# Kernel optimization log

Measured on AMD Instinct MI355X. Metric: run time of the kernel, lower is better.

The kernel has to match this reference:

```python
import jax, jax.numpy as jnp
import numpy as np
import math

B, T, D, H = 4, 1024, 1024, 16
DK = D // H
TAU_THRESH = 0.3


def setup_inputs() -> dict:
    key = jax.random.key(0)
    ks = jax.random.split(key, 13)
    s = 1.0 / math.sqrt(D)
    return {
        "x": jax.random.normal(ks[0], (B, T, D), dtype=jnp.float32),
        "Wq": jax.random.normal(ks[1], (D, D), dtype=jnp.float32) * s,
        "bq": jax.random.normal(ks[2], (D,), dtype=jnp.float32) * s,
        "Wk": jax.random.normal(ks[3], (D, D), dtype=jnp.float32) * s,
        "bk": jax.random.normal(ks[4], (D,), dtype=jnp.float32) * s,
        "Wv": jax.random.normal(ks[5], (D, D), dtype=jnp.float32) * s,
        "bv": jax.random.normal(ks[6], (D,), dtype=jnp.float32) * s,
        "Wo": jax.random.normal(ks[7], (D, D), dtype=jnp.float32) * s,
        "bo": jax.random.normal(ks[8], (D,), dtype=jnp.float32) * s,
        "Wg1": jax.random.normal(ks[9], (1, D), dtype=jnp.float32) * s,
        "bg1": jax.random.normal(ks[10], (1,), dtype=jnp.float32) * s,
        "Wg2": jax.random.normal(ks[11], (1, D), dtype=jnp.float32) * s,
        "bg2": jax.random.normal(ks[12], (1,), dtype=jnp.float32) * s,
    }


def reference(x, Wq, bq, Wk, bk, Wv, bv, Wo, bo, Wg1, bg1, Wg2, bg2):
    b, t, d = x.shape
    # projections (torch Linear: y = x @ W.T + b)
    Q = (x @ Wq.T + bq).reshape(b, t, H, DK).transpose(0, 2, 1, 3)  # [B,H,T,dk]
    K = (x @ Wk.T + bk).reshape(b, t, H, DK).transpose(0, 2, 1, 3)
    V = (x @ Wv.T + bv).reshape(b, t, H, DK).transpose(0, 2, 1, 3)
    scores = jnp.einsum("bhqd,bhkd->bhqk", Q, K) / math.sqrt(DK)  # [B,H,T,T]
    # confidence gates from first-token query context [B, H*dk] = [B, D]
    context = Q[:, :, 0, :].reshape(b, d)
    q1 = jax.nn.sigmoid(context @ Wg1.T + bg1)  # [B,1]
    q2 = jax.nn.sigmoid(context @ Wg2.T + bg2)  # [B,1]
    c = jnp.clip(q1 * q2, 1e-8, 1.0)            # [B,1]
    tau = jnp.where(c < TAU_THRESH, 1.0 / c, jnp.ones_like(c)).reshape(b, 1, 1, 1)
    p = jax.nn.softmax(scores / tau, axis=-1)
    cb = c.reshape(b, 1, 1, 1)
    p_gated = cb * p + (1.0 - cb) * (1.0 / t)
    u = jnp.mean(1.0 - c, axis=-1, keepdims=True)  # [B,1]
    attn_out = jnp.einsum("bhqk,bhkd->bhqd", p_gated, V)
    attn_out = attn_out.transpose(0, 2, 1, 3).reshape(b, t, d)
    output = attn_out @ Wo.T + bo
    return output, u
```

## Files before the change

kernel.cpp:

```cpp
#include <hip/hip_runtime.h>
#include <stdint.h>

typedef short bf16x8 __attribute__((ext_vector_type(8)));
typedef float f32x4 __attribute__((ext_vector_type(4)));

#define MFMA_BF16(a, b, c) __builtin_amdgcn_mfma_f32_16x16x32_bf16((a), (b), (c), 0, 0, 0)

__device__ __forceinline__ short f2bf(float x) {
  union { float f; uint32_t u; } v; v.f = x;
  uint32_t r = (v.u + 0x7FFFu + ((v.u >> 16) & 1u)) >> 16;
  return (short)r;
}
__device__ __forceinline__ uint32_t rnd_bf_hi(float x) {
  union { float f; uint32_t u; } v; v.f = x;
  return v.u + 0x7FFFu + ((v.u >> 16) & 1u);
}
__device__ __forceinline__ uint32_t pack2bf(float a, float b) {
  return __builtin_amdgcn_perm(rnd_bf_hi(b), rnd_bf_hi(a), 0x07060302);
}
__device__ __forceinline__ float bfbits2f(uint32_t b16) {
  union { uint32_t u; float f; } v; v.u = b16 << 16; return v.f;
}
__device__ __forceinline__ float fexp2(float x) {
#if __has_builtin(__builtin_amdgcn_exp2f)
  return __builtin_amdgcn_exp2f(x);
#else
  return __expf(x * 0.6931471805599453f);
#endif
}
__device__ __forceinline__ void async16(const void* g, void* l) {
  __builtin_amdgcn_global_load_lds(
      (const __attribute__((address_space(1))) uint32_t*)g,
      (__attribute__((address_space(3))) uint32_t*)l, 16, 0, 0);
}

#define BAR() __builtin_amdgcn_s_barrier()
#define LGKM0() asm volatile("s_waitcnt lgkmcnt(0)" ::: "memory")
#define VMCNT(n) asm volatile("s_waitcnt vmcnt(" #n ")" ::: "memory")
#define PRIO1() __builtin_amdgcn_s_setprio(1)
#define PRIO0() __builtin_amdgcn_s_setprio(0)

__global__ __launch_bounds__(256) void prep_k(
    const float* __restrict__ x, const float* __restrict__ Wq,
    const float* __restrict__ Wk, const float* __restrict__ Wv,
    const float* __restrict__ Wo, const float* __restrict__ bq,
    short* __restrict__ xb, short* __restrict__ Wqb, short* __restrict__ Wkb,
    short* __restrict__ Wvb, short* __restrict__ Wob, float* __restrict__ ctx) {
  __shared__ float xs[1024];
  const int bid = blockIdx.x;
  const int tid = threadIdx.x;
  if (bid < 8192) {
    const float* src; short* dst; int idx;
    if (bid < 4096) {
      src = x; dst = xb; idx = (bid << 8) + tid;
    } else {
      const int r = bid - 4096;
      const int z = r >> 10;
      src = (z == 0) ? Wq : (z == 1) ? Wk : (z == 2) ? Wv : Wo;
      dst = (z == 0) ? Wqb : (z == 1) ? Wkb : (z == 2) ? Wvb : Wob;
      idx = ((r & 1023) << 8) + tid;
    }
    float4 v = ((const float4*)src)[idx];
    short4 o;
    o.x = f2bf(v.x); o.y = f2bf(v.y); o.z = f2bf(v.z); o.w = f2bf(v.w);
    ((short4*)dst)[idx] = o;
  } else {
    const int r = bid - 8192;
    const int b = r >> 4;
    const int n0 = (r & 15) << 6;
    for (int i = tid; i < 1024; i += 256) xs[i] = x[b * 1048576 + i];
    __syncthreads();
    const int w = tid >> 6, lane = tid & 63;
    const float4* xv4 = (const float4*)xs;
    for (int rr = 0; rr < 16; ++rr) {
      const int n = n0 + (w << 4) + rr;
      const float4* wrow = (const float4*)(Wq + n * 1024);
      float p = 0.f;
#pragma unroll
      for (int c2 = 0; c2 < 4; ++c2) {
        float4 wv = wrow[lane + (c2 << 6)];
        float4 xv = xv4[lane + (c2 << 6)];
        p += xv.x * wv.x + xv.y * wv.y + xv.z * wv.z + xv.w * wv.w;
      }
#pragma unroll
      for (int off = 32; off; off >>= 1) p += __shfl_xor(p, off);
      if (lane == 0) ctx[b * 1024 + n] = p + bq[n];
    }
  }
}

__global__ __launch_bounds__(256) void gates_fin(const float* __restrict__ ctx,
                                                 const float* __restrict__ Wg1,
                                                 const float* __restrict__ bg1,
                                                 const float* __restrict__ Wg2,
                                                 const float* __restrict__ bg2,
                                                 float* __restrict__ gates,
                                                 float* __restrict__ u_out) {
  __shared__ float red[16];
  const int tid = threadIdx.x, w = tid >> 6, lane = tid & 63;
  for (int b = 0; b < 4; ++b) {
    float4 cv = ((const float4*)(ctx + b * 1024))[tid];
    float4 w1 = ((const float4*)Wg1)[tid];
    float4 w2 = ((const float4*)Wg2)[tid];
    float p1 = cv.x * w1.x + cv.y * w1.y + cv.z * w1.z + cv.w * w1.w;
    float p2 = cv.x * w2.x + cv.y * w2.y + cv.z * w2.z + cv.w * w2.w;
#pragma unroll
    for (int off = 32; off; off >>= 1) { p1 += __shfl_xor(p1, off); p2 += __shfl_xor(p2, off); }
    if (lane == 0) { red[w] = p1; red[8 + w] = p2; }
    __syncthreads();
    if (tid == 0) {
      float g1 = red[0] + red[1] + red[2] + red[3] + bg1[0];
      float g2 = red[8] + red[9] + red[10] + red[11] + bg2[0];
      float q1 = 1.f / (1.f + expf(-g1));
      float q2 = 1.f / (1.f + expf(-g2));
      float c = fminf(fmaxf(q1 * q2, 1e-8f), 1.0f);
      gates[b * 2 + 0] = c;
      gates[b * 2 + 1] = (c < 0.3f ? c : 1.0f) * 0.125f * 1.4426950408889634f;
      u_out[b] = 1.0f - c;
    }
    __syncthreads();
  }
}

template <bool SWP>
__device__ __forceinline__ void qkv_core(const short* __restrict__ xb,
                                         const short* __restrict__ W,
                                         const float* __restrict__ bias,
                                         short* __restrict__ out,
                                         short* sm, int m0, int nl0) {
  const int tid = threadIdx.x;
  const int wid = tid >> 6, lane = tid & 63;
  const int wr = wid >> 2, wc = wid & 3;
  const int m15 = lane & 15, quad = lane >> 4;
  const int swz = m15 & 7;

  const int rowb = tid >> 3;
  const int cs = ((tid & 7) ^ (rowb & 7)) << 3;
  const short* aB = xb + (m0 + rowb) * 1024 + cs;
  const short* bB = W + (nl0 + rowb) * 1024 + cs;

  short* As = sm;
  short* Bs = sm + 32768;

#define STAGEH(sb, tt, hf, dst)                        \
  do {                                                 \
    const short* _s = (sb) + (hf)*131072 + (tt)*64;    \
    short* _d = (dst) + ((hf) << 13) + (tid << 3);     \
    async16(_s, _d);                                   \
    async16(_s + 65536, _d + 4096);                    \
  } while (0)

#define RD(base, f, kk)                                                        \
  (*(const bf16x8*)((base) + ((f) << 10) + (m15 << 6) +                        \
                    (((((kk) << 2) + quad) ^ swz) << 3)))

#define MM(accr, af, bf)                                   \
  do {                                                     \
    if (SWP) accr = MFMA_BF16((bf), (af), (accr));         \
    else     accr = MFMA_BF16((af), (bf), (accr));         \
  } while (0)

  f32x4 acc[8][4];
#pragma unroll
  for (int i = 0; i < 8; ++i)
#pragma unroll
    for (int j = 0; j < 4; ++j) { f32x4 zz = {0.f, 0.f, 0.f, 0.f}; acc[i][j] = zz; }

  STAGEH(bB, 0, 0, Bs);
  STAGEH(aB, 0, 0, As);
  STAGEH(aB, 0, 1, As);
  STAGEH(bB, 0, 1, Bs);
  STAGEH(bB, 1, 0, Bs + 16384);
  STAGEH(aB, 1, 0, As + 16384);
  VMCNT(4);
  BAR();

  bf16x8 a[4][2], b0[2][2], b1[2][2];

  for (int t = 0; t < 16; ++t) {
    const int buf = t & 1;
    const short* Ab = As + (buf << 14) + (wr << 13);
    const short* Bb = Bs + (buf << 14) + ((wc >> 1) << 13) + ((wc & 1) << 12);
    short* Adn = As + ((buf ^ 1) << 14);
    short* Bdn = Bs + ((buf ^ 1) << 14);
    short* Ad2 = As + (buf << 14);
    short* Bd2 = Bs + (buf << 14);

#pragma unroll
    for (int fi = 0; fi < 4; ++fi) { a[fi][0] = RD(Ab, fi, 0); a[fi][1] = RD(Ab, fi, 1); }
#pragma unroll
    for (int fj = 0; fj < 2; ++fj) { b0[fj][0] = RD(Bb, fj, 0); b0[fj][1] = RD(Bb, fj, 1); }
    if (t < 15) STAGEH(aB, t + 1, 1, Adn);
    BAR();
    LGKM0();
    PRIO1();
#pragma unroll
    for (int fi = 0; fi < 4; ++fi)
#pragma unroll
      for (int fj = 0; fj < 2; ++fj) {
        MM(acc[fi][fj], a[fi][0], b0[fj][0]);
        MM(acc[fi][fj], a[fi][1], b0[fj][1]);
      }
    PRIO0();
    BAR();

#pragma unroll
    for (int fj = 0; fj < 2; ++fj) { b1[fj][0] = RD(Bb, 2 + fj, 0); b1[fj][1] = RD(Bb, 2 + fj, 1); }
    if (t < 15) STAGEH(bB, t + 1, 1, Bdn);
    BAR();
    LGKM0();
    PRIO1();
#pragma unroll
    for (int fi = 0; fi < 4; ++fi)
#pragma unroll
      for (int fj = 0; fj < 2; ++fj) {
        MM(acc[fi][2 + fj], a[fi][0], b1[fj][0]);
        MM(acc[fi][2 + fj], a[fi][1], b1[fj][1]);
      }
    PRIO0();
    BAR();

#pragma unroll
    for (int fi = 0; fi < 4; ++fi) { a[fi][0] = RD(Ab, 4 + fi, 0); a[fi][1] = RD(Ab, 4 + fi, 1); }
    if (t < 14) STAGEH(bB, t + 2, 0, Bd2);
    BAR();
    LGKM0();
    PRIO1();
#pragma unroll
    for (int fi = 0; fi < 4; ++fi)
#pragma unroll
      for (int fj = 0; fj < 2; ++fj) {
        MM(acc[4 + fi][2 + fj], a[fi][0], b1[fj][0]);
        MM(acc[4 + fi][2 + fj], a[fi][1], b1[fj][1]);
      }
    PRIO0();
    BAR();

    if (t < 14) STAGEH(aB, t + 2, 0, Ad2);
    BAR();
    PRIO1();
#pragma unroll
    for (int fi = 0; fi < 4; ++fi)
#pragma unroll
      for (int fj = 0; fj < 2; ++fj) {
        MM(acc[4 + fi][fj], a[fi][0], b0[fj][0]);
        MM(acc[4 + fi][fj], a[fi][1], b0[fj][1]);
      }
    PRIO0();
    if (t < 14) { VMCNT(4); }
    else if (t == 14) { VMCNT(0); }
    BAR();
  }

  const int nw = nl0 + (wc << 6);
  if (SWP) {
#pragma unroll
    for (int fj = 0; fj < 4; ++fj) {
      const int n = nw + (fj << 4) + (quad << 2);
      const float4 bv = *(const float4*)(bias + n);
      const int hh = n >> 6, dk0 = n & 63;
#pragma unroll
      for (int fi = 0; fi < 8; ++fi) {
        const int m = m0 + (wr << 7) + (fi << 4) + m15;
        const int bb = m >> 10, tt = m & 1023;
        uint2 st;
        st.x = pack2bf(acc[fi][fj][0] + bv.x, acc[fi][fj][1] + bv.y);
        st.y = pack2bf(acc[fi][fj][2] + bv.z, acc[fi][fj][3] + bv.w);
        *(uint2*)(out + (((bb << 4) + hh) << 16) + (tt << 6) + dk0) = st;
      }
    }
  } else {
#pragma unroll
    for (int fj = 0; fj < 4; ++fj) {
      const int n = nw + (fj << 4) + m15;
      const float bv = bias[n];
      const int hh = n >> 6, dk = n & 63;
#pragma unroll
      for (int fi = 0; fi < 8; ++fi) {
        const int m = m0 + (wr << 7) + (fi << 4) + (quad << 2);
        const int bb = m >> 10, t0 = m & 1023;
        uint2 st;
        st.x = pack2bf(acc[fi][fj][0] + bv, acc[fi][fj][1] + bv);
        st.y = pack2bf(acc[fi][fj][2] + bv, acc[fi][fj][3] + bv);
        *(uint2*)(out + (((bb << 4) + hh) << 16) + (dk << 10) + t0) = st;
      }
    }
  }
#undef STAGEH
#undef RD
#undef MM
}

__global__ __launch_bounds__(512) void gemm_qkv8(
    const short* __restrict__ xb,
    const short* __restrict__ Wqb, const short* __restrict__ Wkb, const short* __restrict__ Wvb,
    const float* __restrict__ bq, const float* __restrict__ bk, const float* __restrict__ bv,
    short* __restrict__ Qh, short* __restrict__ Kh, short* __restrict__ Vt) {
  const int lin = blockIdx.x;
  const int s = ((lin & 7) * 24) + (lin >> 3);
  const int bx = s & 15, by = s >> 4;
  const int z = by >> 2;
  const int m0 = bx << 8, nl0 = (by & 3) << 8;
  extern __shared__ short sm[];
  if (z == 0)      qkv_core<true >(xb, Wqb, bq, Qh, sm, m0, nl0);
  else if (z == 1) qkv_core<true >(xb, Wkb, bk, Kh, sm, m0, nl0);
  else             qkv_core<false>(xb, Wvb, bv, Vt, sm, m0, nl0);
}

__global__ __launch_bounds__(256) void gemm_out(const short* __restrict__ Ab,
                                                const short* __restrict__ Wo,
                                                const float* __restrict__ bo,
                                                float* __restrict__ Cout) {
  const int m0 = blockIdx.x << 6;
  const int n0 = blockIdx.y << 7;
  const int tid = threadIdx.x;
  const int w = tid >> 6, lane = tid & 63;
  const int m15 = lane & 15, quad = lane >> 4;
  const int wr = w >> 1, wc = w & 1;

  __shared__ short As[2048];
  __shared__ short Bs[4096];

  f32x4 acc[2][4];
#pragma unroll
  for (int i = 0; i < 2; ++i)
#pragma unroll
    for (int j = 0; j < 4; ++j) { f32x4 zz = {0.f, 0.f, 0.f, 0.f}; acc[i][j] = zz; }

  const int s0 = tid, s1 = tid + 256;
  const int arow = s0 >> 2, alcb = (s0 & 3) ^ ((arow >> 1) & 3);
  const int brow1 = s1 >> 2, blcb1 = (s1 & 3) ^ ((brow1 >> 1) & 3);
  const short* gA  = Ab + (m0 + arow) * 1024 + (alcb << 3);
  const short* gB0 = Wo + (n0 + arow) * 1024 + (alcb << 3);
  const short* gB1 = Wo + (n0 + brow1) * 1024 + (blcb1 << 3);
  short* lA  = &As[s0 << 3];
  short* lB0 = &Bs[s0 << 3];
  short* lB1 = &Bs[s1 << 3];

  for (int kt = 0; kt < 32; ++kt) {
    async16(gA, lA);
    async16(gB0, lB0); async16(gB1, lB1);
    gA += 32; gB0 += 32; gB1 += 32;
    __syncthreads();
    bf16x8 a[2], b[4];
#pragma unroll
    for (int i = 0; i < 2; ++i) {
      const int ra = (wr << 5) + (i << 4) + m15;
      a[i] = *(const bf16x8*)(&As[ra * 32 + ((quad ^ ((ra >> 1) & 3)) << 3)]);
    }
#pragma unroll
    for (int j = 0; j < 4; ++j) {
      const int rb = (wc << 6) + (j << 4) + m15;
      b[j] = *(const bf16x8*)(&Bs[rb * 32 + ((quad ^ ((rb >> 1) & 3)) << 3)]);
    }
#pragma unroll
    for (int i = 0; i < 2; ++i)
#pragma unroll
      for (int j = 0; j < 4; ++j)
        acc[i][j] = MFMA_BF16(a[i], b[j], acc[i][j]);
    __syncthreads();
  }

#pragma unroll
  for (int j = 0; j < 4; ++j) {
    const int n = n0 + (wc << 6) + (j << 4) + m15;
    const float bb_ = bo[n];
#pragma unroll
    for (int i = 0; i < 2; ++i) {
      const int mb = m0 + (wr << 5) + (i << 4) + (quad << 2);
#pragma unroll
      for (int r = 0; r < 4; ++r)
        Cout[(mb + r) * 1024 + n] = acc[i][j][r] + bb_;
    }
  }
}

__global__ __launch_bounds__(256) void meanv_k(const short* __restrict__ Vt,
                                               float* __restrict__ mV) {
  const int bh = blockIdx.x;
  const int tid = threadIdx.x;
  const int d = tid >> 2, part = tid & 3;
  const short* row = Vt + bh * 65536 + d * 1024 + part * 256;
  float s = 0.f;
#pragma unroll 4
  for (int i = 0; i < 64; ++i) {
    uint2 v = *(const uint2*)(row + i * 4);
    s += bfbits2f(v.x & 0xffffu) + bfbits2f(v.x >> 16) +
         bfbits2f(v.y & 0xffffu) + bfbits2f(v.y >> 16);
  }
  s += __shfl_xor(s, 1);
  s += __shfl_xor(s, 2);
  if (part == 0) mV[bh * 64 + d] = s;
}

__global__ __launch_bounds__(256, 2) void attn_k(const short* __restrict__ Qh,
                                                 const short* __restrict__ Kh,
                                                 const short* __restrict__ Vt,
                                                 const float* __restrict__ gates,
                                                 const float* __restrict__ mV,
                                                 short* __restrict__ attnb) {
  const int bh = blockIdx.x;
  const int b = bh >> 4, h = bh & 15;
  const int q0 = blockIdx.y << 7;
  const int tid = threadIdx.x;
  const int w = tid >> 6, lane = tid & 63;
  const int m15 = lane & 15, quad = lane >> 4;

  __shared__ short Ks[2][4096];
  __shared__ short Vs[2][4096];

  const short* ksrc = Kh + bh * 65536;
  const short* vsrc = Vt + bh * 65536;

  const float sl = gates[b * 2 + 1];

  const short* qsrcA = Qh + ((bh << 10) + q0 + (w << 4) + m15) * 64;
  const short* qsrcB = qsrcA + 64 * 64;
  const bf16x8 qA0 = *(const bf16x8*)(qsrcA + (quad << 3));
  const bf16x8 qA1 = *(const bf16x8*)(qsrcA + 32 + (quad << 3));
  const bf16x8 qB0 = *(const bf16x8*)(qsrcB + (quad << 3));
  const bf16x8 qB1 = *(const bf16x8*)(qsrcB + 32 + (quad << 3));

  const int off0 = tid, off1 = tid + 256;
  const int r0 = off0 >> 3, cb0 = (off0 & 7) ^ (r0 & 7);
  const int r1 = off1 >> 3, cb1 = (off1 & 7) ^ (r1 & 7);

#define STAGE(kv, bufi)                                                        \
  do {                                                                         \
    async16(ksrc + (((kv) << 6) + r0) * 64 + (cb0 << 3), &Ks[bufi][off0 << 3]);\
    async16(ksrc + (((kv) << 6) + r1) * 64 + (cb1 << 3), &Ks[bufi][off1 << 3]);\
    async16(vsrc + r0 * 1024 + ((kv) << 6) + (cb0 << 3), &Vs[bufi][off0 << 3]);\
    async16(vsrc + r1 * 1024 + ((kv) << 6) + (cb1 << 3), &Vs[bufi][off1 << 3]);\
  } while (0)

  STAGE(0, 0);

  float lsumA = 0.f, lsumB = 0.f;
  f32x4 oA[4], oB[4];
#pragma unroll
  for (int jd = 0; jd < 4; ++jd) {
    f32x4 zz = {0.f, 0.f, 0.f, 0.f};
    oA[jd] = zz; oB[jd] = zz;
  }

  const int srcA = ((quad & 1) << 5) + m15;
  const int srcB = srcA + 16;
  const bool selhi = (quad & 2) != 0;

#define BUILD_PF(pf, pk)                                                       \
  do {                                                                         \
    _Pragma("unroll")                                                          \
    for (int Hh = 0; Hh < 2; ++Hh) {                                           \
      uint32_t f[4];                                                           \
      _Pragma("unroll")                                                        \
      for (int rp = 0; rp < 2; ++rp) {                                         \
        uint32_t alo = (uint32_t)__shfl((int)pk[2 * Hh][rp], srcA);            \
        uint32_t ahi = (uint32_t)__shfl((int)pk[2 * Hh + 1][rp], srcA);        \
        uint32_t blo = (uint32_t)__shfl((int)pk[2 * Hh][rp], srcB);            \
        uint32_t bhi = (uint32_t)__shfl((int)pk[2 * Hh + 1][rp], srcB);        \
        f[rp]     = selhi ? ahi : alo;                                         \
        f[2 + rp] = selhi ? bhi : blo;                                         \
      }                                                                        \
      pf[Hh] = *(bf16x8*)f;                                                    \
    }                                                                          \
  } while (0)

  for (int kv = 0; kv < 16; ++kv) {
    __syncthreads();
    if (kv < 15) STAGE(kv + 1, (kv + 1) & 1);
    const short* Kb = &Ks[kv & 1][0];
    const short* Vb = &Vs[kv & 1][0];

    f32x4 sA[4], sB[4];
#pragma unroll
    for (int s = 0; s < 4; ++s) {
      const int row = (s << 4) + m15;
      const int sw = row & 7;
      bf16x8 a0 = *(const bf16x8*)(Kb + (row << 6) + ((quad ^ sw) << 3));
      bf16x8 a1 = *(const bf16x8*)(Kb + (row << 6) + (((quad + 4) ^ sw) << 3));
      f32x4 zA = {0.f, 0.f, 0.f, 0.f};
      zA = MFMA_BF16(a0, qA0, zA);
      zA = MFMA_BF16(a1, qA1, zA);
      sA[s] = zA;
      f32x4 zB = {0.f, 0.f, 0.f, 0.f};
      zB = MFMA_BF16(a0, qB0, zB);
      zB = MFMA_BF16(a1, qB1, zB);
      sB[s] = zB;
    }

    uint32_t pkA[4][2], pkB[4][2];
#pragma unroll
    for (int s = 0; s < 4; ++s) {
      float a0 = fexp2(sA[s][0] * sl);
      float a1 = fexp2(sA[s][1] * sl);
      float a2 = fexp2(sA[s][2] * sl);
      float a3 = fexp2(sA[s][3] * sl);
      lsumA += (a0 + a1) + (a2 + a3);
      pkA[s][0] = pack2bf(a0, a1);
      pkA[s][1] = pack2bf(a2, a3);
      float b0 = fexp2(sB[s][0] * sl);
      float b1 = fexp2(sB[s][1] * sl);
      float b2 = fexp2(sB[s][2] * sl);
      float b3 = fexp2(sB[s][3] * sl);
      lsumB += (b0 + b1) + (b2 + b3);
      pkB[s][0] = pack2bf(b0, b1);
      pkB[s][1] = pack2bf(b2, b3);
    }

    bf16x8 pfA[2], pfB[2];
    BUILD_PF(pfA, pkA);
    BUILD_PF(pfB, pkB);

#pragma unroll
    for (int jd = 0; jd < 4; ++jd) {
      const int row = (jd << 4) + m15;
      const int sw = row & 7;
      bf16x8 v0 = *(const bf16x8*)(Vb + (row << 6) + ((quad ^ sw) << 3));
      bf16x8 v1 = *(const bf16x8*)(Vb + (row << 6) + (((quad + 4) ^ sw) << 3));
      oA[jd] = MFMA_BF16(v0, pfA[0], oA[jd]);
      oA[jd] = MFMA_BF16(v1, pfA[1], oA[jd]);
      oB[jd] = MFMA_BF16(v0, pfB[0], oB[jd]);
      oB[jd] = MFMA_BF16(v1, pfB[1], oB[jd]);
    }
  }
#undef STAGE
#undef BUILD_PF

  float lA = lsumA;
  lA += __shfl_xor(lA, 16);
  lA += __shfl_xor(lA, 32);
  float lB = lsumB;
  lB += __shfl_xor(lB, 16);
  lB += __shfl_xor(lB, 32);

  const float cg = gates[b * 2 + 0];
  const float sc0A = cg / lA;
  const float sc0B = cg / lB;
  const float coef = (1.0f - cg) * (1.0f / 1024.0f);
  const int qrowA = q0 + (w << 4) + m15;
  short* orowA = attnb + ((b << 10) + qrowA) * 1024 + (h << 6);
  short* orowB = orowA + 64 * 1024;
#pragma unroll
  for (int jd = 0; jd < 4; ++jd) {
    float4 mv = *(const float4*)(mV + (bh << 6) + (jd << 4) + (quad << 2));
    uint2 stA;
    stA.x = pack2bf(sc0A * oA[jd][0] + coef * mv.x, sc0A * oA[jd][1] + coef * mv.y);
    stA.y = pack2bf(sc0A * oA[jd][2] + coef * mv.z, sc0A * oA[jd][3] + coef * mv.w);
    *(uint2*)(orowA + (jd << 4) + (quad << 2)) = stA;
    uint2 stB;
    stB.x = pack2bf(sc0B * oB[jd][0] + coef * mv.x, sc0B * oB[jd][1] + coef * mv.y);
    stB.y = pack2bf(sc0B * oB[jd][2] + coef * mv.z, sc0B * oB[jd][3] + coef * mv.w);
    *(uint2*)(orowB + (jd << 4) + (quad << 2)) = stB;
  }
}

extern "C" void kernel_launch(void* const* d_in, const int* in_sizes, int n_in,
                              void* d_out, int out_size, void* d_ws, size_t ws_size,
                              hipStream_t stream) {
  const float* x   = (const float*)d_in[0];
  const float* Wq  = (const float*)d_in[1];
  const float* bq  = (const float*)d_in[2];
  const float* Wk  = (const float*)d_in[3];
  const float* bk  = (const float*)d_in[4];
  const float* Wv  = (const float*)d_in[5];
  const float* bv  = (const float*)d_in[6];
  const float* Wo  = (const float*)d_in[7];
  const float* bo  = (const float*)d_in[8];
  const float* Wg1 = (const float*)d_in[9];
  const float* bg1 = (const float*)d_in[10];
  const float* Wg2 = (const float*)d_in[11];
  const float* bg2 = (const float*)d_in[12];
  float* out = (float*)d_out;

  char* ws = (char*)d_ws;
  short* xb   = (short*)(ws + 0);
  short* Wqb  = (short*)(ws + 8388608);
  short* Wkb  = (short*)(ws + 10485760);
  short* Wvb  = (short*)(ws + 12582912);
  short* Wob  = (short*)(ws + 14680064);
  short* Qh   = (short*)(ws + 16777216);
  short* Kh   = (short*)(ws + 25165824);
  short* Vt   = (short*)(ws + 33554432);
  short* attb = (short*)(ws + 41943040);
  float* ctx  = (float*)(ws + 50331648);
  float* gat  = (float*)(ws + 50348032);
  float* mV   = (float*)(ws + 50348064);

  static bool lds_inited = false;
  if (!lds_inited) {
    hipFuncSetAttribute(reinterpret_cast<const void*>(gemm_qkv8),
                        hipFuncAttributeMaxDynamicSharedMemorySize, 131072);
    lds_inited = true;
  }

  prep_k<<<8256, 256, 0, stream>>>(x, Wq, Wk, Wv, Wo, bq,
                                   xb, Wqb, Wkb, Wvb, Wob, ctx);
  gates_fin<<<1, 256, 0, stream>>>(ctx, Wg1, bg1, Wg2, bg2, gat, out + 4194304);

  gemm_qkv8<<<192, 512, 131072, stream>>>(xb, Wqb, Wkb, Wvb, bq, bk, bv,
                                          Qh, Kh, Vt);
  meanv_k<<<64, 256, 0, stream>>>(Vt, mV);
  attn_k<<<dim3(64, 8), 256, 0, stream>>>(Qh, Kh, Vt, gat, mV, attb);
  gemm_out<<<dim3(64, 8), 256, 0, stream>>>(attb, Wob, bo, out);
}
```

Baseline: 211.7 us.

## Fuse V mean into attention via MFMA, enlarge out-GEMM tile, change LDS swizzle

Drops the separate meanv kernel and computes the V column sums inside the attention kernel with extra MFMAs against a ones vector. This removes a launch and a pass over Vt, at the cost of two more MFMAs per PV step. The output GEMM tile grows from 64x128 to 128x128, halving the grid and raising per-block reuse, and its LDS swizzle is removed. The QKV GEMM swizzle is changed to a simpler XOR pattern, which may raise LDS bank conflicts.

```diff
diff --git a/kernel.cpp b/kernel.cpp
--- a/kernel.cpp
+++ b/kernel.cpp
@@ -132,12 +132,11 @@
   const int wid = tid >> 6, lane = tid & 63;
   const int wr = wid >> 2, wc = wid & 3;
   const int m15 = lane & 15, quad = lane >> 4;
-  const int swz = m15 & 7;
 
   const int rowb = tid >> 3;
-  const int cs = ((tid & 7) ^ (rowb & 7)) << 3;
-  const short* aB = xb + (m0 + rowb) * 1024 + cs;
-  const short* bB = W + (nl0 + rowb) * 1024 + cs;
+  const int c16 = (tid & 7) ^ (((tid >> 5) & 1) << 1);
+  const short* aB = xb + (m0 + rowb) * 1024 + (c16 << 3);
+  const short* bB = W + (nl0 + rowb) * 1024 + (c16 << 3);
 
   short* As = sm;
   short* Bs = sm + 32768;
@@ -152,7 +151,7 @@
 
 #define RD(base, f, kk)                                                        \
   (*(const bf16x8*)((base) + ((f) << 10) + (m15 << 6) +                        \
-                    (((((kk) << 2) + quad) ^ swz) << 3)))
+                    (((((kk) << 2) + quad) ^ ((m15 & 4) >> 1)) << 3)))
 
 #define MM(accr, af, bf)                                   \
   do {                                                     \
@@ -311,50 +310,47 @@
                                                 const short* __restrict__ Wo,
                                                 const float* __restrict__ bo,
                                                 float* __restrict__ Cout) {
-  const int m0 = blockIdx.x << 6;
+  const int m0 = blockIdx.x << 7;
   const int n0 = blockIdx.y << 7;
   const int tid = threadIdx.x;
   const int w = tid >> 6, lane = tid & 63;
   const int m15 = lane & 15, quad = lane >> 4;
   const int wr = w >> 1, wc = w & 1;
 
-  __shared__ short As[2048];
+  __shared__ short As[4096];
   __shared__ short Bs[4096];
 
-  f32x4 acc[2][4];
-#pragma unroll
-  for (int i = 0; i < 2; ++i)
+  f32x4 acc[4][4];
+#pragma unroll
+  for (int i = 0; i < 4; ++i)
 #pragma unroll
     for (int j = 0; j < 4; ++j) { f32x4 zz = {0.f, 0.f, 0.f, 0.f}; acc[i][j] = zz; }
 
-  const int s0 = tid, s1 = tid + 256;
-  const int arow = s0 >> 2, alcb = (s0 & 3) ^ ((arow >> 1) & 3);
-  const int brow1 = s1 >> 2, blcb1 = (s1 & 3) ^ ((brow1 >> 1) & 3);
-  const short* gA  = Ab + (m0 + arow) * 1024 + (alcb << 3);
-  const short* gB0 = Wo + (n0 + arow) * 1024 + (alcb << 3);
-  const short* gB1 = Wo + (n0 + brow1) * 1024 + (blcb1 << 3);
-  short* lA  = &As[s0 << 3];
-  short* lB0 = &Bs[s0 << 3];
-  short* lB1 = &Bs[s1 << 3];
+  const int srow = (w << 5) + (lane >> 2);
+  const int scol = (lane & 3) << 3;
+  const short* ga0 = Ab + (m0 + srow) * 1024 + scol;
+  const short* ga1 = ga0 + 16 * 1024;
+  const short* gb0 = Wo + (n0 + srow) * 1024 + scol;
+  const short* gb1 = gb0 + 16 * 1024;
+  short* la0 = &As[srow * 32 + scol];
+  short* la1 = la0 + 512;
+  short* lb0 = &Bs[srow * 32 + scol];
+  short* lb1 = lb0 + 512;
 
   for (int kt = 0; kt < 32; ++kt) {
-    async16(gA, lA);
-    async16(gB0, lB0); async16(gB1, lB1);
-    gA += 32; gB0 += 32; gB1 += 32;
+    async16(ga0, la0); async16(ga1, la1);
+    async16(gb0, lb0); async16(gb1, lb1);
+    ga0 += 32; ga1 += 32; gb0 += 32; gb1 += 32;
     __syncthreads();
-    bf16x8 a[2], b[4];
-#pragma unroll
-    for (int i = 0; i < 2; ++i) {
-      const int ra = (wr << 5) + (i << 4) + m15;
-      a[i] = *(const bf16x8*)(&As[ra * 32 + ((quad ^ ((ra >> 1) & 3)) << 3)]);
-    }
-#pragma unroll
-    for (int j = 0; j < 4; ++j) {
-      const int rb = (wc << 6) + (j << 4) + m15;
-      b[j] = *(const bf16x8*)(&Bs[rb * 32 + ((quad ^ ((rb >> 1) & 3)) << 3)]);
-    }
-#pragma unroll
-    for (int i = 0; i < 2; ++i)
+    bf16x8 a[4], b[4];
+#pragma unroll
+    for (int i = 0; i < 4; ++i)
+      a[i] = *(const bf16x8*)(&As[((wr << 6) + (i << 4) + m15) * 32 + (quad << 3)]);
+#pragma unroll
+    for (int j = 0; j < 4; ++j)
+      b[j] = *(const bf16x8*)(&Bs[((wc << 6) + (j << 4) + m15) * 32 + (quad << 3)]);
+#pragma unroll
+    for (int i = 0; i < 4; ++i)
 #pragma unroll
       for (int j = 0; j < 4; ++j)
         acc[i][j] = MFMA_BF16(a[i], b[j], acc[i][j]);
@@ -366,38 +362,19 @@
     const int n = n0 + (wc << 6) + (j << 4) + m15;
     const float bb_ = bo[n];
 #pragma unroll
-    for (int i = 0; i < 2; ++i) {
-      const int mb = m0 + (wr << 5) + (i << 4) + (quad << 2);
+    for (int i = 0; i < 4; ++i) {
+      const int mb = m0 + (wr << 6) + (i << 4) + (quad << 2);
 #pragma unroll
       for (int r = 0; r < 4; ++r)
         Cout[(mb + r) * 1024 + n] = acc[i][j][r] + bb_;
     }
   }
-}
-
-__global__ __launch_bounds__(256) void meanv_k(const short* __restrict__ Vt,
-                                               float* __restrict__ mV) {
-  const int bh = blockIdx.x;
-  const int tid = threadIdx.x;
-  const int d = tid >> 2, part = tid & 3;
-  const short* row = Vt + bh * 65536 + d * 1024 + part * 256;
-  float s = 0.f;
-#pragma unroll 4
-  for (int i = 0; i < 64; ++i) {
-    uint2 v = *(const uint2*)(row + i * 4);
-    s += bfbits2f(v.x & 0xffffu) + bfbits2f(v.x >> 16) +
-         bfbits2f(v.y & 0xffffu) + bfbits2f(v.y >> 16);
-  }
-  s += __shfl_xor(s, 1);
-  s += __shfl_xor(s, 2);
-  if (part == 0) mV[bh * 64 + d] = s;
 }
 
 __global__ __launch_bounds__(256, 2) void attn_k(const short* __restrict__ Qh,
                                                  const short* __restrict__ Kh,
                                                  const short* __restrict__ Vt,
                                                  const float* __restrict__ gates,
-                                                 const float* __restrict__ mV,
                                                  short* __restrict__ attnb) {
   const int bh = blockIdx.x;
   const int b = bh >> 4, h = bh & 15;
@@ -421,6 +398,8 @@
   const bf16x8 qB0 = *(const bf16x8*)(qsrcB + (quad << 3));
   const bf16x8 qB1 = *(const bf16x8*)(qsrcB + 32 + (quad << 3));
 
+  const bf16x8 vone = {0x3F80, 0x3F80, 0x3F80, 0x3F80, 0x3F80, 0x3F80, 0x3F80, 0x3F80};
+
   const int off0 = tid, off1 = tid + 256;
   const int r0 = off0 >> 3, cb0 = (off0 & 7) ^ (r0 & 7);
   const int r1 = off1 >> 3, cb1 = (off1 & 7) ^ (r1 & 7);
@@ -436,11 +415,11 @@
   STAGE(0, 0);
 
   float lsumA = 0.f, lsumB = 0.f;
-  f32x4 oA[4], oB[4];
+  f32x4 oA[4], oB[4], o_mv[4];
 #pragma unroll
   for (int jd = 0; jd < 4; ++jd) {
     f32x4 zz = {0.f, 0.f, 0.f, 0.f};
-    oA[jd] = zz; oB[jd] = zz;
+    oA[jd] = zz; oB[jd] = zz; o_mv[jd] = zz;
   }
 
   const int srcA = ((quad & 1) << 5) + m15;
@@ -521,6 +500,8 @@
       oA[jd] = MFMA_BF16(v1, pfA[1], oA[jd]);
       oB[jd] = MFMA_BF16(v0, pfB[0], oB[jd]);
       oB[jd] = MFMA_BF16(v1, pfB[1], oB[jd]);
+      o_mv[jd] = MFMA_BF16(v0, vone, o_mv[jd]);
+      o_mv[jd] = MFMA_BF16(v1, vone, o_mv[jd]);
     }
   }
 #undef STAGE
@@ -542,14 +523,17 @@
   short* orowB = orowA + 64 * 1024;
 #pragma unroll
   for (int jd = 0; jd < 4; ++jd) {
-    float4 mv = *(const float4*)(mV + (bh << 6) + (jd << 4) + (quad << 2));
     uint2 stA;
-    stA.x = pack2bf(sc0A * oA[jd][0] + coef * mv.x, sc0A * oA[jd][1] + coef * mv.y);
-    stA.y = pack2bf(sc0A * oA[jd][2] + coef * mv.z, sc0A * oA[jd][3] + coef * mv.w);
+    stA.x = pack2bf(sc0A * oA[jd][0] + coef * o_mv[jd][0],
+                    sc0A * oA[jd][1] + coef * o_mv[jd][1]);
+    stA.y = pack2bf(sc0A * oA[jd][2] + coef * o_mv[jd][2],
+                    sc0A * oA[jd][3] + coef * o_mv[jd][3]);
     *(uint2*)(orowA + (jd << 4) + (quad << 2)) = stA;
     uint2 stB;
-    stB.x = pack2bf(sc0B * oB[jd][0] + coef * mv.x, sc0B * oB[jd][1] + coef * mv.y);
-    stB.y = pack2bf(sc0B * oB[jd][2] + coef * mv.z, sc0B * oB[jd][3] + coef * mv.w);
+    stB.x = pack2bf(sc0B * oB[jd][0] + coef * o_mv[jd][0],
+                    sc0B * oB[jd][1] + coef * o_mv[jd][1]);
+    stB.y = pack2bf(sc0B * oB[jd][2] + coef * o_mv[jd][2],
+                    sc0B * oB[jd][3] + coef * o_mv[jd][3]);
     *(uint2*)(orowB + (jd << 4) + (quad << 2)) = stB;
   }
 }
@@ -584,7 +568,6 @@
   short* attb = (short*)(ws + 41943040);
   float* ctx  = (float*)(ws + 50331648);
   float* gat  = (float*)(ws + 50348032);
-  float* mV   = (float*)(ws + 50348064);
 
   static bool lds_inited = false;
   if (!lds_inited) {
@@ -599,7 +582,6 @@
 
   gemm_qkv8<<<192, 512, 131072, stream>>>(xb, Wqb, Wkb, Wvb, bq, bk, bv,
                                           Qh, Kh, Vt);
-  meanv_k<<<64, 256, 0, stream>>>(Vt, mV);
-  attn_k<<<dim3(64, 8), 256, 0, stream>>>(Qh, Kh, Vt, gat, mV, attb);
-  gemm_out<<<dim3(64, 8), 256, 0, stream>>>(attb, Wob, bo, out);
-}
+  attn_k<<<dim3(64, 8), 256, 0, stream>>>(Qh, Kh, Vt, gat, attb);
+  gemm_out<<<dim3(32, 8), 256, 0, stream>>>(attb, Wob, bo, out);
+}
```

After: 213.8 us. About the same (+1.0%).
